# Performance work log

Measured on AMD Instinct MI355X. Metric: run time of the kernel, lower is better.

The kernel has to match this reference:

```python
import jax, jax.numpy as jnp
import numpy as np

N, E, D, H, LAYERS = 50000, 800000, 128, 8, 2
LRELU_ALPHA = 0.2


def _seg_softmax(logits, seg, n):
    # numerically stable softmax over edges grouped by destination node
    m = jax.ops.segment_max(logits, seg, num_segments=n)
    z = jnp.exp(logits - m[seg])
    s = jax.ops.segment_sum(z, seg, num_segments=n)
    return z / jnp.maximum(s[seg], 1e-16)


def _gat_layer(x, src, dst, W, a_src, a_dst, concat):
    # W: [H, Fin, F'], a_src/a_dst: [H, F']
    n = x.shape[0]
    outs = []
    for h in range(W.shape[0]):  # loop over heads to bound peak memory
        Wh = x @ W[h]                              # [N, F']
        es = Wh @ a_src[h]                         # [N]
        ed = Wh @ a_dst[h]                         # [N]
        e = jax.nn.leaky_relu(es[src] + ed[dst], LRELU_ALPHA)  # [E]
        att = _seg_softmax(e, dst, n)              # [E]
        out = jax.ops.segment_sum(att[:, None] * Wh[src], dst, num_segments=n)
        outs.append(out)
    if concat:
        return jax.nn.elu(jnp.concatenate(outs, axis=-1))  # [N, H*F']
    return jnp.mean(jnp.stack(outs, axis=0), axis=0)        # [N, F']


def _rel_gcn_layer(x, src, dst, w, W):
    # weighted-adjacency GCN with row (in-degree) normalization + ReLU
    n = x.shape[0]
    deg = jax.ops.segment_sum(w, dst, num_segments=n)
    norm = w / jnp.maximum(deg[dst], 1e-16)        # [E]
    h = x @ W                                      # [N, Dout]
    agg = jax.ops.segment_sum(norm[:, None] * h[src], dst, num_segments=n)
    return jax.nn.relu(agg)


def setup_inputs() -> dict:
    key = jax.random.key(0)
    ks = jax.random.split(key, 12)
    s = 1.0 / np.sqrt(D)
    return {
        "x": jax.random.normal(ks[0], (N, D), dtype=jnp.float32),
        "edge_index": jax.random.randint(ks[1], (2, E), 0, N, dtype=jnp.int64),
        "edge_weight": jax.random.uniform(ks[2], (E,), dtype=jnp.float32),
        "gat_W0": jax.random.normal(ks[3], (H, D, D // H), dtype=jnp.float32) * s,
        "gat_a0_src": jax.random.normal(ks[4], (H, D // H), dtype=jnp.float32) * s,
        "gat_a0_dst": jax.random.normal(ks[5], (H, D // H), dtype=jnp.float32) * s,
        "gat_W1": jax.random.normal(ks[6], (H, D, D), dtype=jnp.float32) * s,
        "gat_a1_src": jax.random.normal(ks[7], (H, D), dtype=jnp.float32) * s,
        "gat_a1_dst": jax.random.normal(ks[8], (H, D), dtype=jnp.float32) * s,
        "gcn_W0": jax.random.normal(ks[9], (D, D), dtype=jnp.float32) * s,
        "gcn_W1": jax.random.normal(ks[10], (D, D), dtype=jnp.float32) * s,
    }


def reference(x, edge_index, edge_weight, gat_W0, gat_a0_src, gat_a0_dst,
              gat_W1, gat_a1_src, gat_a1_dst, gcn_W0, gcn_W1):
    src, dst = edge_index[0], edge_index[1]
    gat_params = [(gat_W0, gat_a0_src, gat_a0_dst), (gat_W1, gat_a1_src, gat_a1_dst)]
    gcn_params = [gcn_W0, gcn_W1]
    x1, x2 = x, x  # dropout is identity in eval mode
    for i in range(LAYERS):
        W, a_s, a_d = gat_params[i]
        x1 = _gat_layer(x1, src, dst, W, a_s, a_d, concat=(i != LAYERS - 1))
        x2 = _rel_gcn_layer(x2, src, dst, edge_weight, gcn_params[i])
    # cat along new last dim then MaxPool1d(2) == elementwise max of branches
    return jnp.maximum(x1, x2)
```

## Files before the change

### kernel.cpp

```cpp
#include <hip/hip_runtime.h>

#define LRELU_ALPHA 0.2f

typedef __attribute__((ext_vector_type(8))) short short8;
typedef __attribute__((ext_vector_type(4))) float float4v;
typedef __attribute__((ext_vector_type(2))) float f32x2;

__device__ __forceinline__ unsigned short f2bf(float f) {
  union { float f; unsigned u; } x; x.f = f;
  unsigned r = (x.u + 0x7fff + ((x.u >> 16) & 1)) >> 16;
  return (unsigned short)r;
}
__device__ __forceinline__ float bflo(unsigned u) {
  union { unsigned u; float f; } x; x.u = u << 16; return x.f;
}
__device__ __forceinline__ float bfhi(unsigned u) {
  union { unsigned u; float f; } x; x.u = u & 0xffff0000u; return x.f;
}
__device__ __forceinline__ f32x2 bfpair(unsigned u) {
  return (f32x2){bflo(u), bfhi(u)};
}
__device__ __forceinline__ unsigned packbf(float a, float b) {
  return (unsigned)f2bf(a) | ((unsigned)f2bf(b) << 16);
}


__global__ __launch_bounds__(256) void k_count(const int* __restrict__ dst,
                                               int* __restrict__ cnt, int E) {
  int e = blockIdx.x * 256 + threadIdx.x;
  if (e < E) atomicAdd(&cnt[dst[e]], 1);
}

__global__ __launch_bounds__(1024) void k_scan1(const int* __restrict__ cnt,
                                                int* __restrict__ lscan,
                                                int* __restrict__ bsum, int N) {
  __shared__ int sm[1024];
  int t = threadIdx.x;
  int base = blockIdx.x * 1024;
  int v = (base + t < N) ? cnt[base + t] : 0;
  sm[t] = v;
  __syncthreads();
  for (int off = 1; off < 1024; off <<= 1) {
    int x = (t >= off) ? sm[t - off] : 0;
    __syncthreads();
    sm[t] += x;
    __syncthreads();
  }
  if (base + t < N) lscan[base + t] = sm[t] - v;
  if (t == 1023) bsum[blockIdx.x] = sm[1023];
}

__global__ __launch_bounds__(64) void k_scan2(int* __restrict__ bsum,
                                              int* __restrict__ rowptrN, int nb) {
  int t = threadIdx.x;
  int v = (t < nb) ? bsum[t] : 0;
  int orig = v;
  for (int off = 1; off < 64; off <<= 1) {
    int y = __shfl_up(v, off, 64);
    if (t >= off) v += y;
  }
  if (t < nb) bsum[t] = v - orig;
  if (t == 63) *rowptrN = v;
}

__global__ __launch_bounds__(1024) void k_scan3(int* __restrict__ rowptr,
                                                int* __restrict__ cur,
                                                const int* __restrict__ bsum, int N) {
  int i = blockIdx.x * 1024 + threadIdx.x;
  if (i < N) {
    int v = rowptr[i] + bsum[blockIdx.x];
    rowptr[i] = v;
    cur[i] = v;
  }
}

__global__ __launch_bounds__(256) void k_scatter(const int* __restrict__ src,
                                                 const int* __restrict__ dst,
                                                 const float* __restrict__ w,
                                                 int* __restrict__ cur,
                                                 uint2* __restrict__ edata, int E) {
  int base = (blockIdx.x * 256 + threadIdx.x) * 4;
  if (base >= E) return;
  int n = E - base; if (n > 4) n = 4;
  int ss[4], dd[4]; float ww[4];
  if (n == 4) {
    int4 s4 = *(const int4*)(src + base);
    int4 d4 = *(const int4*)(dst + base);
    float4 w4 = *(const float4*)(w + base);
    ss[0] = s4.x; ss[1] = s4.y; ss[2] = s4.z; ss[3] = s4.w;
    dd[0] = d4.x; dd[1] = d4.y; dd[2] = d4.z; dd[3] = d4.w;
    ww[0] = w4.x; ww[1] = w4.y; ww[2] = w4.z; ww[3] = w4.w;
  } else {
    for (int i = 0; i < n; ++i) { ss[i] = src[base + i]; dd[i] = dst[base + i]; ww[i] = w[base + i]; }
  }
  int pp[4];
#pragma unroll
  for (int i = 0; i < 4; ++i)
    if (i < n) pp[i] = atomicAdd(&cur[dd[i]], 1);
#pragma unroll
  for (int i = 0; i < 4; ++i)
    if (i < n) edata[pp[i]] = make_uint2((unsigned)ss[i], __float_as_uint(ww[i]));
}

__global__ __launch_bounds__(256) void k_pack(const float* __restrict__ W0,
                                              const float* __restrict__ a0s,
                                              const float* __restrict__ a0d,
                                              const float* __restrict__ W1,
                                              const float* __restrict__ a1s,
                                              const float* __restrict__ a1d,
                                              const float* __restrict__ gw0,
                                              const float* __restrict__ gw1,
                                              unsigned short* __restrict__ W0catT,
                                              float* __restrict__ logitW,
                                              unsigned short* __restrict__ gw1T,
                                              unsigned short* __restrict__ va1T,
                                              unsigned short* __restrict__ WstackT) {
  int idx = blockIdx.x * 256 + threadIdx.x;
  if (idx < 32768) {
    int n = idx >> 7, k = idx & 127;
    float v;
    if (n < 128) {
      int h = n >> 4, f = n & 15;
      v = W0[h * 2048 + k * 16 + f];
    } else {
      v = gw0[k * 128 + (n - 128)];
    }
    W0catT[idx] = f2bf(v);
  } else if (idx < 34816) {
    int j = idx - 32768;
    int k = j >> 4, c = j & 15;
    int h = (c < 8) ? c : c - 8;
    const float* a = (c < 8) ? a0s : a0d;
    float s = 0.f;
    for (int f = 0; f < 16; ++f) s += W0[h * 2048 + k * 16 + f] * a[h * 16 + f];
    logitW[j] = s;
  } else if (idx < 51200) {
    int j = idx - 34816;
    int n = j >> 7, k = j & 127;
    gw1T[j] = f2bf(gw1[k * 128 + n]);
  } else if (idx < 53248) {
    int j = idx - 51200;
    int c = j >> 7, k = j & 127;
    int h = c & 7;
    const float* a = (c < 8) ? a1s : a1d;
    float s = 0.f;
    for (int f = 0; f < 128; ++f) s += W1[h * 16384 + k * 128 + f] * a[h * 128 + f];
    va1T[j] = f2bf(s);
  } else if (idx < 184320) {
    int j = idx - 53248;
    int n = j >> 10, kk = j & 1023;
    int h = kk >> 7, k = kk & 127;
    WstackT[j] = f2bf(W1[h * 16384 + k * 128 + n] * 0.125f);
  }
}

__global__ __launch_bounds__(256) void k_prep(const float* __restrict__ x,
                                              const float* __restrict__ logitW,
                                              unsigned short* __restrict__ xb,
                                              float* __restrict__ logit0, int N) {
  __shared__ float sm[16][132];
  __shared__ float sw[2048];
  int t = threadIdx.x;
  int base = blockIdx.x * 16;
  int r = t >> 4, cc = (t & 15) * 8;
  const float* xr = x + (size_t)(base + r) * 128 + cc;
  float4 v0 = *(const float4*)xr;
  float4 v1 = *(const float4*)(xr + 4);
  ushort4 o0 = {f2bf(v0.x), f2bf(v0.y), f2bf(v0.z), f2bf(v0.w)};
  ushort4 o1 = {f2bf(v1.x), f2bf(v1.y), f2bf(v1.z), f2bf(v1.w)};
  *(ushort4*)(xb + (size_t)(base + r) * 128 + cc) = o0;
  *(ushort4*)(xb + (size_t)(base + r) * 128 + cc + 4) = o1;
  *(float4*)&sm[r][cc] = v0;
  *(float4*)&sm[r][cc + 4] = v1;
  *(float4*)&sw[t * 8] = *(const float4*)(logitW + t * 8);
  *(float4*)&sw[t * 8 + 4] = *(const float4*)(logitW + t * 8 + 4);
  __syncthreads();
  int c = t & 15;
  float acc = 0.f;
#pragma unroll
  for (int k = 0; k < 128; ++k) acc += sm[r][k] * sw[k * 16 + c];
  logit0[(size_t)(base + r) * 16 + c] = acc;
}

template <int NT, int OUT_BF16, int EPI>
__global__ __launch_bounds__(256) void k_mgemm(const unsigned short* __restrict__ A, int lda,
                                               const unsigned short* __restrict__ BT, int ldb,
                                               void* __restrict__ Cv, int ldc,
                                               const void* __restrict__ aux,
                                               int M, int Ncols, int K) {
  __shared__ unsigned short As[64][64];
  __shared__ unsigned short Bs[NT * 16][64];
  int tid = threadIdx.x;
  int w = tid >> 6, lane = tid & 63;
  int quad = lane >> 4, l16 = lane & 15;
  int row0 = blockIdx.x * 64;
  int c0 = blockIdx.y * (NT * 16);
  float4v acc[NT];
#pragma unroll
  for (int t = 0; t < NT; ++t) acc[t] = (float4v){0.f, 0.f, 0.f, 0.f};

  for (int k0 = 0; k0 < K; k0 += 64) {
    __syncthreads();
#pragma unroll
    for (int i = 0; i < 2; ++i) {
      int c = tid + i * 256;
      int r = c >> 3, kc = c & 7;
      uint4 v = {0u, 0u, 0u, 0u};
      int gr = row0 + r;
      if (gr < M) v = *(const uint4*)(A + (size_t)gr * lda + k0 + kc * 8);
      *(uint4*)(&As[r][(kc ^ (r & 7)) * 8]) = v;
    }
#pragma unroll
    for (int i = 0; i < (NT * 128 + 255) / 256; ++i) {
      int c = tid + i * 256;
      if (c < NT * 128) {
        int n = c >> 3, kc = c & 7;
        uint4 v = {0u, 0u, 0u, 0u};
        int gn = c0 + n;
        if (gn < Ncols) v = *(const uint4*)(BT + (size_t)gn * ldb + k0 + kc * 8);
        *(uint4*)(&Bs[n][(kc ^ (n & 7)) * 8]) = v;
      }
    }
    __syncthreads();
#pragma unroll
    for (int ks = 0; ks < 2; ++ks) {
      int m = w * 16 + l16;
      int ga = (ks * 4 + quad) ^ (m & 7);
      short8 a = *(const short8*)(&As[m][ga * 8]);
#pragma unroll
      for (int t = 0; t < NT; ++t) {
        int n = t * 16 + l16;
        int gb = (ks * 4 + quad) ^ (n & 7);
        short8 b = *(const short8*)(&Bs[n][gb * 8]);
        acc[t] = __builtin_amdgcn_mfma_f32_16x16x32_bf16(a, b, acc[t], 0, 0, 0);
      }
    }
  }
#pragma unroll
  for (int t = 0; t < NT; ++t) {
    int cc = c0 + t * 16 + l16;
    if (cc >= Ncols) continue;
#pragma unroll
    for (int i = 0; i < 4; ++i) {
      int rr = row0 + w * 16 + quad * 4 + i;
      if (rr >= M) continue;
      float v = acc[t][i];
      if (EPI == 1) {
        unsigned short us = ((const unsigned short*)aux)[(size_t)rr * ldc + cc];
        v = fmaxf(v, bflo((unsigned)us));
      }
      if (EPI == 5) v = fmaxf(v, 0.f);
      if (EPI == 4) {
        if (cc < 128) {
          ((unsigned short*)Cv)[(size_t)rr * 192 + cc] = f2bf(v);
        } else {
          int enc = __builtin_amdgcn_cvt_pk_fp8_f32(v, v, 0, false);
          ((unsigned char*)aux)[(size_t)rr * 384 + 256 + (cc - 128)] = (unsigned char)(enc & 0xff);
        }
      } else if (OUT_BF16)
        ((unsigned short*)Cv)[(size_t)rr * ldc + cc] = f2bf(v);
      else
        ((float*)Cv)[(size_t)rr * ldc + cc] = v;
    }
  }
}

__global__ __launch_bounds__(256, 8) void k_agg0(const unsigned short* __restrict__ feat,
                                                 const int* __restrict__ rowptr,
                                                 const uint2* __restrict__ edata,
                                                 const float* __restrict__ logit0,
                                                 unsigned short* __restrict__ xh, int N) {
  __shared__ uint2 swl[4][64];
  __shared__ float pl[4][512];
  __shared__ __align__(16) float lnv[4][8];
  int wave = threadIdx.x >> 6, lane = threadIdx.x & 63;
  int head = lane >> 3, h8 = lane & 7, e8 = lane >> 3;
  const char* FG = (const char*)feat + lane * 4;
  const char* FC = (const char*)feat + 256 + lane * 2;
  for (int d = blockIdx.x * 4 + wave; d < N; d += gridDim.x * 4) {
    int beg = rowptr[d], end = rowptr[d + 1], deg = end - beg;
    float edv = logit0[(size_t)d * 16 + 8 + h8];
    f32x2 aa = {0.f, 0.f}, ga = {0.f, 0.f};
    float lsum = 0.f, wsum = 0.f;
    for (int base = 0; base < deg; base += 64) {
      int idx = beg + base + lane;
      uint2 sv = make_uint2(0u, 0u);
      if (idx < end) sv = edata[idx];
      swl[wave][lane] = sv;
      int ng = deg - base; if (ng > 64) ng = 64;
#pragma unroll
      for (int j = 0; j < 8; ++j) {
        int e = j * 8 + e8;
        unsigned s = swl[wave][e].x;
        float es = logit0[(size_t)s * 16 + h8];
        float lg = es + edv;
        lg = lg > 0.f ? lg : LRELU_ALPHA * lg;
        float p = (e < ng) ? __expf(fminf(lg, 80.f)) : 0.f;
        pl[wave][j * 64 + lane] = p;
        lsum += p;
      }
      int t = 0;
      for (; t + 4 <= ng; t += 4) {
        uint2 s0 = swl[wave][t], s1 = swl[wave][t + 1];
        uint2 s2 = swl[wave][t + 2], s3 = swl[wave][t + 3];
        unsigned g0 = *(const unsigned*)(FG + (size_t)s0.x * 384);
        unsigned g1 = *(const unsigned*)(FG + (size_t)s1.x * 384);
        unsigned g2 = *(const unsigned*)(FG + (size_t)s2.x * 384);
        unsigned g3 = *(const unsigned*)(FG + (size_t)s3.x * 384);
        unsigned c0 = *(const unsigned short*)(FC + (size_t)s0.x * 384);
        unsigned c1 = *(const unsigned short*)(FC + (size_t)s1.x * 384);
        unsigned c2 = *(const unsigned short*)(FC + (size_t)s2.x * 384);
        unsigned c3 = *(const unsigned short*)(FC + (size_t)s3.x * 384);
        float p0 = pl[wave][t * 8 + head];
        float p1 = pl[wave][t * 8 + 8 + head];
        float p2 = pl[wave][t * 8 + 16 + head];
        float p3 = pl[wave][t * 8 + 24 + head];
        float w0 = __uint_as_float(s0.y), w1 = __uint_as_float(s1.y);
        float w2 = __uint_as_float(s2.y), w3 = __uint_as_float(s3.y);
        aa += bfpair(g0) * p0; ga += __builtin_amdgcn_cvt_pk_f32_fp8(c0, false) * w0; wsum += w0;
        aa += bfpair(g1) * p1; ga += __builtin_amdgcn_cvt_pk_f32_fp8(c1, false) * w1; wsum += w1;
        aa += bfpair(g2) * p2; ga += __builtin_amdgcn_cvt_pk_f32_fp8(c2, false) * w2; wsum += w2;
        aa += bfpair(g3) * p3; ga += __builtin_amdgcn_cvt_pk_f32_fp8(c3, false) * w3; wsum += w3;
      }
      for (; t < ng; ++t) {
        uint2 s0 = swl[wave][t];
        unsigned g0 = *(const unsigned*)(FG + (size_t)s0.x * 384);
        unsigned c0 = *(const unsigned short*)(FC + (size_t)s0.x * 384);
        float p0 = pl[wave][t * 8 + head];
        float w0 = __uint_as_float(s0.y);
        aa += bfpair(g0) * p0; ga += __builtin_amdgcn_cvt_pk_f32_fp8(c0, false) * w0; wsum += w0;
      }
    }
    lsum += __shfl_xor(lsum, 8, 64);
    lsum += __shfl_xor(lsum, 16, 64);
    lsum += __shfl_xor(lsum, 32, 64);
    if (lane < 8) lnv[wave][lane] = lsum > 0.f ? 1.f / lsum : 0.f;
    float inv = lnv[wave][head];
    float v0 = aa.x * inv, v1 = aa.y * inv;
    v0 = v0 > 0.f ? v0 : __expf(v0) - 1.f;
    v1 = v1 > 0.f ? v1 : __expf(v1) - 1.f;
    char* xr = (char*)xh + (size_t)d * 512;
    *(unsigned*)(xr + lane * 4) = packbf(v0, v1);
    float ginv = 1.f / fmaxf(wsum, 1e-16f);
    *(unsigned*)(xr + 256 + lane * 4) =
        packbf(fmaxf(ga.x * ginv, 0.f), fmaxf(ga.y * ginv, 0.f));
  }
}

__global__ __launch_bounds__(256, 8) void k_agg1(const unsigned short* __restrict__ xh,
                                                 const float* __restrict__ esed,
                                                 const int* __restrict__ rowptr,
                                                 const uint2* __restrict__ edata,
                                                 unsigned short* __restrict__ aggbuf,
                                                 unsigned short* __restrict__ x2a, int N) {
  __shared__ uint2 swl[4][64];
  __shared__ float pl[4][512];
  __shared__ __align__(16) float lnv[4][8];
  int wave = threadIdx.x >> 6, lane = threadIdx.x & 63;
  int h8 = lane & 7, e8 = lane >> 3;
  const char* XG = (const char*)xh + lane * 4;
  const char* XC = (const char*)xh + 256 + lane * 4;
  for (int d = blockIdx.x * 4 + wave; d < N; d += gridDim.x * 4) {
    int beg = rowptr[d], end = rowptr[d + 1], deg = end - beg;
    float edv = esed[(size_t)d * 16 + 8 + h8];
    f32x2 axp[8] = {};
    f32x2 gp = {0.f, 0.f};
    float lsum = 0.f, wsum = 0.f;
#define EDGE1(u1, u2, ss, tt)                                \
  {                                                          \
    float4 pv0 = *(const float4*)&pl[wave][(tt) * 8];        \
    float4 pv1 = *(const float4*)&pl[wave][(tt) * 8 + 4];    \
    float wj = __uint_as_float((ss).y);                      \
    f32x2 xA = bfpair(u1);                                   \
    f32x2 hA = bfpair(u2);                                   \
    axp[0] += xA * pv0.x; axp[1] += xA * pv0.y;              \
    axp[2] += xA * pv0.z; axp[3] += xA * pv0.w;              \
    axp[4] += xA * pv1.x; axp[5] += xA * pv1.y;              \
    axp[6] += xA * pv1.z; axp[7] += xA * pv1.w;              \
    gp += hA * wj; wsum += wj;                               \
  }
    for (int base = 0; base < deg; base += 64) {
      int idx = beg + base + lane;
      uint2 sv = make_uint2(0u, 0u);
      if (idx < end) sv = edata[idx];
      swl[wave][lane] = sv;
      int ng = deg - base; if (ng > 64) ng = 64;
#pragma unroll
      for (int j = 0; j < 8; ++j) {
        int e = j * 8 + e8;
        unsigned s = swl[wave][e].x;
        float es = esed[(size_t)s * 16 + h8];
        float lg = es + edv;
        lg = lg > 0.f ? lg : LRELU_ALPHA * lg;
        float p = (e < ng) ? __expf(fminf(lg, 80.f)) : 0.f;
        pl[wave][j * 64 + lane] = p;
        lsum += p;
      }
      int t = 0;
      for (; t + 4 <= ng; t += 4) {
        uint2 s0 = swl[wave][t], s1 = swl[wave][t + 1];
        uint2 s2 = swl[wave][t + 2], s3 = swl[wave][t + 3];
        unsigned a0 = *(const unsigned*)(XG + (size_t)s0.x * 512);
        unsigned a1 = *(const unsigned*)(XG + (size_t)s1.x * 512);
        unsigned a2 = *(const unsigned*)(XG + (size_t)s2.x * 512);
        unsigned a3 = *(const unsigned*)(XG + (size_t)s3.x * 512);
        unsigned b0 = *(const unsigned*)(XC + (size_t)s0.x * 512);
        unsigned b1 = *(const unsigned*)(XC + (size_t)s1.x * 512);
        unsigned b2 = *(const unsigned*)(XC + (size_t)s2.x * 512);
        unsigned b3 = *(const unsigned*)(XC + (size_t)s3.x * 512);
        EDGE1(a0, b0, s0, t)
        EDGE1(a1, b1, s1, t + 1)
        EDGE1(a2, b2, s2, t + 2)
        EDGE1(a3, b3, s3, t + 3)
      }
      for (; t < ng; ++t) {
        uint2 s0 = swl[wave][t];
        unsigned a0 = *(const unsigned*)(XG + (size_t)s0.x * 512);
        unsigned b0 = *(const unsigned*)(XC + (size_t)s0.x * 512);
        EDGE1(a0, b0, s0, t)
      }
    }
#undef EDGE1
    lsum += __shfl_xor(lsum, 8, 64);
    lsum += __shfl_xor(lsum, 16, 64);
    lsum += __shfl_xor(lsum, 32, 64);
    if (lane < 8) lnv[wave][lane] = lsum > 0.f ? 1.f / lsum : 0.f;
    const float4* lp = (const float4*)lnv[wave];
    float4 i0 = lp[0], i1 = lp[1];
    unsigned* ab = (unsigned*)aggbuf + (size_t)d * 512 + lane;
    ab[0]   = packbf(axp[0].x * i0.x, axp[0].y * i0.x);
    ab[64]  = packbf(axp[1].x * i0.y, axp[1].y * i0.y);
    ab[128] = packbf(axp[2].x * i0.z, axp[2].y * i0.z);
    ab[192] = packbf(axp[3].x * i0.w, axp[3].y * i0.w);
    ab[256] = packbf(axp[4].x * i1.x, axp[4].y * i1.x);
    ab[320] = packbf(axp[5].x * i1.y, axp[5].y * i1.y);
    ab[384] = packbf(axp[6].x * i1.z, axp[6].y * i1.z);
    ab[448] = packbf(axp[7].x * i1.w, axp[7].y * i1.w);
    float ginv = 1.f / fmaxf(wsum, 1e-16f);
    ((unsigned*)x2a)[(size_t)d * 64 + lane] = packbf(gp.x * ginv, gp.y * ginv);
  }
}


extern "C" void kernel_launch(void* const* d_in, const int* in_sizes, int n_in,
                              void* d_out, int out_size, void* d_ws, size_t ws_size,
                              hipStream_t stream) {
  const float* x   = (const float*)d_in[0];
  const int*   ei  = (const int*)d_in[1];
  const float* ew  = (const float*)d_in[2];
  const float* W0  = (const float*)d_in[3];
  const float* a0s = (const float*)d_in[4];
  const float* a0d = (const float*)d_in[5];
  const float* W1  = (const float*)d_in[6];
  const float* a1s = (const float*)d_in[7];
  const float* a1d = (const float*)d_in[8];
  const float* gw0 = (const float*)d_in[9];
  const float* gw1 = (const float*)d_in[10];
  float* out = (float*)d_out;

  const int N = in_sizes[0] / 128;
  const int E = in_sizes[1] / 2;
  const int* src = ei;
  const int* dst = ei + E;

  char* p = (char*)d_ws;
  auto carve = [&](size_t bytes) {
    void* r = (void*)p;
    p += (bytes + 255) & ~(size_t)255;
    return r;
  };
  int*   cnt    = (int*)carve((size_t)N * 4);
  int*   rowptr = (int*)carve((size_t)(N + 1) * 4);
  int*   cur    = (int*)carve((size_t)N * 4);
  int*   bsum   = (int*)carve(256 * 4);
  uint2* edata  = (uint2*)carve((size_t)E * 8);
  unsigned short* W0catT  = (unsigned short*)carve(32768 * 2);
  float*          logitW  = (float*)carve(2048 * 4);
  unsigned short* gw1T    = (unsigned short*)carve(16384 * 2);
  unsigned short* va1T    = (unsigned short*)carve(2048 * 2);
  unsigned short* WstackT = (unsigned short*)carve(131072 * 2);
  float*          esed = (float*)carve((size_t)N * 16 * 4);
  unsigned short* xh   = (unsigned short*)carve((size_t)N * 512);
  unsigned short* x2a  = (unsigned short*)carve((size_t)N * 128 * 2);
  size_t ph1 = ((size_t)N * 128 * 2 + 255) & ~(size_t)255;
  size_t ph2 = ph1 + (((size_t)N * 384 + 255) & ~(size_t)255);
  size_t ph3 = ph2 + (((size_t)N * 16 * 4 + 255) & ~(size_t)255);
  size_t scratch_sz = (size_t)N * 1024 * 2;
  if (ph3 > scratch_sz) scratch_sz = ph3;
  char* scratch = (char*)carve(scratch_sz);
  unsigned short* xb     = (unsigned short*)scratch;
  unsigned short* feat   = (unsigned short*)(scratch + ph1);
  float*          logit0 = (float*)(scratch + ph2);
  unsigned short* aggbuf = (unsigned short*)scratch;

  int gE = (E + 255) / 256;
  int gE4 = ((E + 3) / 4 + 255) / 256;
  int nb = (N + 1023) / 1024;
  int gM = (N + 63) / 64;
  int gD = (N + 3) / 4;
  int gA = gD < 2048 ? gD : 2048;

  hipMemsetAsync(cnt, 0, (size_t)N * 4, stream);
  k_count<<<gE, 256, 0, stream>>>(dst, cnt, E);
  k_scan1<<<nb, 1024, 0, stream>>>(cnt, rowptr, bsum, N);
  k_scan2<<<1, 64, 0, stream>>>(bsum, rowptr + N, nb);
  k_scan3<<<nb, 1024, 0, stream>>>(rowptr, cur, bsum, N);

  k_scatter<<<gE4, 256, 0, stream>>>(src, dst, ew, cur, edata, E);

  k_pack<<<(184320 + 255) / 256, 256, 0, stream>>>(W0, a0s, a0d, W1, a1s, a1d, gw0,
                                                   gw1, W0catT, logitW, gw1T, va1T,
                                                   WstackT);
  k_prep<<<(N + 15) / 16, 256, 0, stream>>>(x, logitW, xb, logit0, N);

  k_mgemm<8, 1, 4><<<dim3(gM, 2), 256, 0, stream>>>(xb, 128, W0catT, 128, feat, 192,
                                                    feat, N, 256, 128);
  k_agg0<<<gA, 256, 0, stream>>>(feat, rowptr, edata, logit0, xh, N);

  k_mgemm<1, 0, 0><<<dim3(gM, 1), 256, 0, stream>>>(xh, 256, va1T, 128, esed, 16,
                                                    nullptr, N, 16, 128);

  k_agg1<<<gA, 256, 0, stream>>>(xh, esed, rowptr, edata, aggbuf, x2a, N);

  k_mgemm<8, 1, 5><<<dim3(gM, 1), 256, 0, stream>>>(x2a, 128, gw1T, 128, x2a, 128,
                                                    nullptr, N, 128, 128);

  k_mgemm<8, 0, 1><<<dim3(gM, 1), 256, 0, stream>>>(aggbuf, 1024, WstackT, 1024, out,
                                                    128, x2a, N, 128, 1024);
}
```

Measured before the change: 496.3 us.

## Precompute per-edge attention weights in a separate pass and interleave aggregated features

A new kernel, run before each GAT aggregation, computes the per-edge, per-head exp-logits and stores them as bf16, along with per-node inverse softmax sums. The aggregation kernels then read these precomputed weights instead of gathering source logits and computing exp inline. k_agg0 now writes the GAT and GCN outputs interleaved, so k_agg1 fetches both with a single 8-byte gather per edge. It also writes a compact copy of the GAT half, which becomes the input to the logits GEMM. The cost is an extra E*16-byte write and read of edge weights per layer, two extra launches, and bf16 rounding of the attention weights.

```diff
diff --git a/kernel.cpp b/kernel.cpp
--- a/kernel.cpp
+++ b/kernel.cpp
@@ -182,6 +182,33 @@
   logit0[(size_t)(base + r) * 16 + c] = acc;
 }
 
+__global__ __launch_bounds__(256) void k_pedge(const float* __restrict__ logits,
+                                               const uint2* __restrict__ edata,
+                                               const int* __restrict__ rowptr,
+                                               unsigned short* __restrict__ pedge,
+                                               float* __restrict__ linv, int N) {
+  int wave = threadIdx.x >> 6, lane = threadIdx.x & 63;
+  int d = blockIdx.x * 4 + wave;
+  if (d >= N) return;
+  int j8 = lane >> 3, h = lane & 7;
+  float edv = logits[(size_t)d * 16 + 8 + h];
+  int beg = rowptr[d], end = rowptr[d + 1];
+  float lsum = 0.f;
+  for (int ii = beg + j8; ii < end; ii += 8) {
+    unsigned s = edata[ii].x;
+    float es = logits[(size_t)s * 16 + h];
+    float lg = es + edv;
+    lg = lg > 0.f ? lg : LRELU_ALPHA * lg;
+    float p = __expf(fminf(lg, 80.f));
+    lsum += p;
+    pedge[(size_t)ii * 8 + h] = f2bf(p);
+  }
+  lsum += __shfl_xor(lsum, 8, 64);
+  lsum += __shfl_xor(lsum, 16, 64);
+  lsum += __shfl_xor(lsum, 32, 64);
+  if (lane < 8) linv[(size_t)d * 8 + h] = lsum > 0.f ? 1.f / lsum : 0.f;
+}
+
 template <int NT, int OUT_BF16, int EPI>
 __global__ __launch_bounds__(256) void k_mgemm(const unsigned short* __restrict__ A, int lda,
                                                const unsigned short* __restrict__ BT, int ldb,
@@ -268,37 +295,34 @@
 __global__ __launch_bounds__(256, 8) void k_agg0(const unsigned short* __restrict__ feat,
                                                  const int* __restrict__ rowptr,
                                                  const uint2* __restrict__ edata,
-                                                 const float* __restrict__ logit0,
-                                                 unsigned short* __restrict__ xh, int N) {
+                                                 const unsigned short* __restrict__ pedge,
+                                                 const float* __restrict__ linv,
+                                                 unsigned short* __restrict__ xh,
+                                                 unsigned short* __restrict__ x1cc, int N) {
   __shared__ uint2 swl[4][64];
   __shared__ float pl[4][512];
-  __shared__ __align__(16) float lnv[4][8];
   int wave = threadIdx.x >> 6, lane = threadIdx.x & 63;
-  int head = lane >> 3, h8 = lane & 7, e8 = lane >> 3;
+  int head = lane >> 3;
   const char* FG = (const char*)feat + lane * 4;
   const char* FC = (const char*)feat + 256 + lane * 2;
   for (int d = blockIdx.x * 4 + wave; d < N; d += gridDim.x * 4) {
     int beg = rowptr[d], end = rowptr[d + 1], deg = end - beg;
-    float edv = logit0[(size_t)d * 16 + 8 + h8];
     f32x2 aa = {0.f, 0.f}, ga = {0.f, 0.f};
-    float lsum = 0.f, wsum = 0.f;
+    float wsum = 0.f;
     for (int base = 0; base < deg; base += 64) {
       int idx = beg + base + lane;
       uint2 sv = make_uint2(0u, 0u);
-      if (idx < end) sv = edata[idx];
+      uint4 q = make_uint4(0u, 0u, 0u, 0u);
+      if (idx < end) {
+        sv = edata[idx];
+        q = *(const uint4*)(pedge + (size_t)idx * 8);
+      }
       swl[wave][lane] = sv;
+      float4 pa = make_float4(bflo(q.x), bfhi(q.x), bflo(q.y), bfhi(q.y));
+      float4 pb = make_float4(bflo(q.z), bfhi(q.z), bflo(q.w), bfhi(q.w));
+      *(float4*)&pl[wave][lane * 8] = pa;
+      *(float4*)&pl[wave][lane * 8 + 4] = pb;
       int ng = deg - base; if (ng > 64) ng = 64;
-#pragma unroll
-      for (int j = 0; j < 8; ++j) {
-        int e = j * 8 + e8;
-        unsigned s = swl[wave][e].x;
-        float es = logit0[(size_t)s * 16 + h8];
-        float lg = es + edv;
-        lg = lg > 0.f ? lg : LRELU_ALPHA * lg;
-        float p = (e < ng) ? __expf(fminf(lg, 80.f)) : 0.f;
-        pl[wave][j * 64 + lane] = p;
-        lsum += p;
-      }
       int t = 0;
       for (; t + 4 <= ng; t += 4) {
         uint2 s0 = swl[wave][t], s1 = swl[wave][t + 1];
@@ -331,48 +355,41 @@
         aa += bfpair(g0) * p0; ga += __builtin_amdgcn_cvt_pk_f32_fp8(c0, false) * w0; wsum += w0;
       }
     }
-    lsum += __shfl_xor(lsum, 8, 64);
-    lsum += __shfl_xor(lsum, 16, 64);
-    lsum += __shfl_xor(lsum, 32, 64);
-    if (lane < 8) lnv[wave][lane] = lsum > 0.f ? 1.f / lsum : 0.f;
-    float inv = lnv[wave][head];
+    float inv = linv[(size_t)d * 8 + head];
     float v0 = aa.x * inv, v1 = aa.y * inv;
     v0 = v0 > 0.f ? v0 : __expf(v0) - 1.f;
     v1 = v1 > 0.f ? v1 : __expf(v1) - 1.f;
-    char* xr = (char*)xh + (size_t)d * 512;
-    *(unsigned*)(xr + lane * 4) = packbf(v0, v1);
     float ginv = 1.f / fmaxf(wsum, 1e-16f);
-    *(unsigned*)(xr + 256 + lane * 4) =
-        packbf(fmaxf(ga.x * ginv, 0.f), fmaxf(ga.y * ginv, 0.f));
+    unsigned px = packbf(v0, v1);
+    ((uint2*)xh)[(size_t)d * 64 + lane] =
+        make_uint2(px, packbf(fmaxf(ga.x * ginv, 0.f), fmaxf(ga.y * ginv, 0.f)));
+    ((unsigned*)x1cc)[(size_t)d * 64 + lane] = px;
   }
 }
 
 __global__ __launch_bounds__(256, 8) void k_agg1(const unsigned short* __restrict__ xh,
-                                                 const float* __restrict__ esed,
                                                  const int* __restrict__ rowptr,
                                                  const uint2* __restrict__ edata,
+                                                 const unsigned short* __restrict__ pedge,
+                                                 const float* __restrict__ linv,
                                                  unsigned short* __restrict__ aggbuf,
                                                  unsigned short* __restrict__ x2a, int N) {
   __shared__ uint2 swl[4][64];
   __shared__ float pl[4][512];
-  __shared__ __align__(16) float lnv[4][8];
   int wave = threadIdx.x >> 6, lane = threadIdx.x & 63;
-  int h8 = lane & 7, e8 = lane >> 3;
-  const char* XG = (const char*)xh + lane * 4;
-  const char* XC = (const char*)xh + 256 + lane * 4;
+  const uint2* X2 = (const uint2*)xh + lane;
   for (int d = blockIdx.x * 4 + wave; d < N; d += gridDim.x * 4) {
     int beg = rowptr[d], end = rowptr[d + 1], deg = end - beg;
-    float edv = esed[(size_t)d * 16 + 8 + h8];
     f32x2 axp[8] = {};
     f32x2 gp = {0.f, 0.f};
-    float lsum = 0.f, wsum = 0.f;
-#define EDGE1(u1, u2, ss, tt)                                \
+    float wsum = 0.f;
+#define EDGE1(uu, ss, tt)                                    \
   {                                                          \
     float4 pv0 = *(const float4*)&pl[wave][(tt) * 8];        \
     float4 pv1 = *(const float4*)&pl[wave][(tt) * 8 + 4];    \
     float wj = __uint_as_float((ss).y);                      \
-    f32x2 xA = bfpair(u1);                                   \
-    f32x2 hA = bfpair(u2);                                   \
+    f32x2 xA = bfpair((uu).x);                               \
+    f32x2 hA = bfpair((uu).y);                               \
     axp[0] += xA * pv0.x; axp[1] += xA * pv0.y;              \
     axp[2] += xA * pv0.z; axp[3] += xA * pv0.w;              \
     axp[4] += xA * pv1.x; axp[5] += xA * pv1.y;              \
@@ -382,51 +399,39 @@
     for (int base = 0; base < deg; base += 64) {
       int idx = beg + base + lane;
       uint2 sv = make_uint2(0u, 0u);
-      if (idx < end) sv = edata[idx];
+      uint4 q = make_uint4(0u, 0u, 0u, 0u);
+      if (idx < end) {
+        sv = edata[idx];
+        q = *(const uint4*)(pedge + (size_t)idx * 8);
+      }
       swl[wave][lane] = sv;
+      float4 pa = make_float4(bflo(q.x), bfhi(q.x), bflo(q.y), bfhi(q.y));
+      float4 pb = make_float4(bflo(q.z), bfhi(q.z), bflo(q.w), bfhi(q.w));
+      *(float4*)&pl[wave][lane * 8] = pa;
+      *(float4*)&pl[wave][lane * 8 + 4] = pb;
       int ng = deg - base; if (ng > 64) ng = 64;
-#pragma unroll
-      for (int j = 0; j < 8; ++j) {
-        int e = j * 8 + e8;
-        unsigned s = swl[wave][e].x;
-        float es = esed[(size_t)s * 16 + h8];
-        float lg = es + edv;
-        lg = lg > 0.f ? lg : LRELU_ALPHA * lg;
-        float p = (e < ng) ? __expf(fminf(lg, 80.f)) : 0.f;
-        pl[wave][j * 64 + lane] = p;
-        lsum += p;
-      }
       int t = 0;
       for (; t + 4 <= ng; t += 4) {
         uint2 s0 = swl[wave][t], s1 = swl[wave][t + 1];
         uint2 s2 = swl[wave][t + 2], s3 = swl[wave][t + 3];
-        unsigned a0 = *(const unsigned*)(XG + (size_t)s0.x * 512);
-        unsigned a1 = *(const unsigned*)(XG + (size_t)s1.x * 512);
-        unsigned a2 = *(const unsigned*)(XG + (size_t)s2.x * 512);
-        unsigned a3 = *(const unsigned*)(XG + (size_t)s3.x * 512);
-        unsigned b0 = *(const unsigned*)(XC + (size_t)s0.x * 512);
-        unsigned b1 = *(const unsigned*)(XC + (size_t)s1.x * 512);
-        unsigned b2 = *(const unsigned*)(XC + (size_t)s2.x * 512);
-        unsigned b3 = *(const unsigned*)(XC + (size_t)s3.x * 512);
-        EDGE1(a0, b0, s0, t)
-        EDGE1(a1, b1, s1, t + 1)
-        EDGE1(a2, b2, s2, t + 2)
-        EDGE1(a3, b3, s3, t + 3)
+        uint2 u0 = X2[(size_t)s0.x * 64];
+        uint2 u1 = X2[(size_t)s1.x * 64];
+        uint2 u2 = X2[(size_t)s2.x * 64];
+        uint2 u3 = X2[(size_t)s3.x * 64];
+        EDGE1(u0, s0, t)
+        EDGE1(u1, s1, t + 1)
+        EDGE1(u2, s2, t + 2)
+        EDGE1(u3, s3, t + 3)
       }
       for (; t < ng; ++t) {
         uint2 s0 = swl[wave][t];
-        unsigned a0 = *(const unsigned*)(XG + (size_t)s0.x * 512);
-        unsigned b0 = *(const unsigned*)(XC + (size_t)s0.x * 512);
-        EDGE1(a0, b0, s0, t)
+        uint2 u0 = X2[(size_t)s0.x * 64];
+        EDGE1(u0, s0, t)
       }
     }
 #undef EDGE1
-    lsum += __shfl_xor(lsum, 8, 64);
-    lsum += __shfl_xor(lsum, 16, 64);
-    lsum += __shfl_xor(lsum, 32, 64);
-    if (lane < 8) lnv[wave][lane] = lsum > 0.f ? 1.f / lsum : 0.f;
-    const float4* lp = (const float4*)lnv[wave];
-    float4 i0 = lp[0], i1 = lp[1];
+    float4 i0 = *(const float4*)(linv + (size_t)d * 8);
+    float4 i1 = *(const float4*)(linv + (size_t)d * 8 + 4);
     unsigned* ab = (unsigned*)aggbuf + (size_t)d * 512 + lane;
     ab[0]   = packbf(axp[0].x * i0.x, axp[0].y * i0.x);
     ab[64]  = packbf(axp[1].x * i0.y, axp[1].y * i0.y);
@@ -482,6 +487,8 @@
   float*          esed = (float*)carve((size_t)N * 16 * 4);
   unsigned short* xh   = (unsigned short*)carve((size_t)N * 512);
   unsigned short* x2a  = (unsigned short*)carve((size_t)N * 128 * 2);
+  unsigned short* pedge = (unsigned short*)carve((size_t)E * 8 * 2);
+  float*          linv  = (float*)carve((size_t)N * 8 * 4);
   size_t ph1 = ((size_t)N * 128 * 2 + 255) & ~(size_t)255;
   size_t ph2 = ph1 + (((size_t)N * 384 + 255) & ~(size_t)255);
   size_t ph3 = ph2 + (((size_t)N * 16 * 4 + 255) & ~(size_t)255);
@@ -489,6 +496,7 @@
   if (ph3 > scratch_sz) scratch_sz = ph3;
   char* scratch = (char*)carve(scratch_sz);
   unsigned short* xb     = (unsigned short*)scratch;
+  unsigned short* x1cc   = (unsigned short*)scratch;
   unsigned short* feat   = (unsigned short*)(scratch + ph1);
   float*          logit0 = (float*)(scratch + ph2);
   unsigned short* aggbuf = (unsigned short*)scratch;
@@ -513,14 +521,18 @@
                                                    WstackT);
   k_prep<<<(N + 15) / 16, 256, 0, stream>>>(x, logitW, xb, logit0, N);
 
+  k_pedge<<<gD, 256, 0, stream>>>(logit0, edata, rowptr, pedge, linv, N);
+
   k_mgemm<8, 1, 4><<<dim3(gM, 2), 256, 0, stream>>>(xb, 128, W0catT, 128, feat, 192,
                                                     feat, N, 256, 128);
-  k_agg0<<<gA, 256, 0, stream>>>(feat, rowptr, edata, logit0, xh, N);
-
-  k_mgemm<1, 0, 0><<<dim3(gM, 1), 256, 0, stream>>>(xh, 256, va1T, 128, esed, 16,
+  k_agg0<<<gA, 256, 0, stream>>>(feat, rowptr, edata, pedge, linv, xh, x1cc, N);
+
+  k_mgemm<1, 0, 0><<<dim3(gM, 1), 256, 0, stream>>>(x1cc, 128, va1T, 128, esed, 16,
                                                     nullptr, N, 16, 128);
 
-  k_agg1<<<gA, 256, 0, stream>>>(xh, esed, rowptr, edata, aggbuf, x2a, N);
+  k_pedge<<<gD, 256, 0, stream>>>(esed, edata, rowptr, pedge, linv, N);
+
+  k_agg1<<<gA, 256, 0, stream>>>(xh, rowptr, edata, pedge, linv, aggbuf, x2a, N);
 
   k_mgemm<8, 1, 5><<<dim3(gM, 1), 256, 0, stream>>>(x2a, 128, gw1T, 128, x2a, 128,
                                                     nullptr, N, 128, 128);
```

Measured after the change: 455.5 us. -8.2%, faster.
